# Performance work log

Measured on AMD Instinct MI355X. Metric: run time of the kernel, lower is better.

Reference implementation:

```python
import jax, jax.numpy as jnp
import numpy as np

HIDDEN = 1024
HEADS = 16
D_K = HIDDEN // HEADS
B, S = 2, 2048


def setup_inputs() -> dict:
    key = jax.random.key(0)
    ks = jax.random.split(key, 11)
    sc = 1.0 / np.sqrt(HIDDEN)
    inp = {
        "q": jax.random.normal(ks[0], (B, S, HIDDEN), jnp.float32),
        "k": jax.random.normal(ks[1], (B, S, HIDDEN), jnp.float32),
        "v": jax.random.normal(ks[2], (B, S, HIDDEN), jnp.float32),
        "Wq": jax.random.normal(ks[3], (HIDDEN, HIDDEN), jnp.float32) * sc,
        "bq": jnp.zeros((HIDDEN,), jnp.float32),
        "Wk": jax.random.normal(ks[4], (HIDDEN, HIDDEN), jnp.float32) * sc,
        "bk": jnp.zeros((HIDDEN,), jnp.float32),
        "Wv": jax.random.normal(ks[5], (HIDDEN, HIDDEN), jnp.float32) * sc,
        "bv": jnp.zeros((HIDDEN,), jnp.float32),
        "Wo": jax.random.normal(ks[6], (HIDDEN, HIDDEN), jnp.float32) * sc,
        "bo": jnp.zeros((HIDDEN,), jnp.float32),
    }
    return inp


def reference(q, k, v, Wq, bq, Wk, bk, Wv, bv, Wo, bo):
    bs = q.shape[0]
    # projections; torch Linear: x @ W.T + b
    def proj(x, W, b):
        y = x @ W.T + b  # [B,S,H*Dk]
        return y.reshape(bs, -1, HEADS, D_K).transpose(0, 2, 1, 3)  # [B,h,S,Dk]
    qh, kh, vh = proj(q, Wq, bq), proj(k, Wk, bk), proj(v, Wv, bv)
    scores = jnp.einsum("bhqd,bhkd->bhqk", qh, kh) / jnp.sqrt(jnp.float32(D_K))
    attn = jax.nn.softmax(scores, axis=-1)  # dropout is identity in eval mode
    x = jnp.einsum("bhqk,bhkd->bhqd", attn, vh)
    x = x.transpose(0, 2, 1, 3).reshape(bs, -1, HEADS * D_K)
    return x @ Wo.T + bo
```

## Files before the change

kernel.cpp:

```cpp
#include <hip/hip_runtime.h>
#include <stdint.h>

#define HIDDEN 1024
#define HEADS  16
#define DK     64
#define BATCH  2
#define SEQ    2048
#define MTOT   (BATCH*SEQ)
#define QSCALE 0.1803368801111204f

typedef float  f32x4   __attribute__((ext_vector_type(4)));
typedef float  f32x16  __attribute__((ext_vector_type(16)));
typedef __bf16 bf16x8  __attribute__((ext_vector_type(8)));

__device__ __forceinline__ unsigned short f2bf(float f) {
    union { float f; uint32_t u; } x;
    x.f = f;
    uint32_t r = x.u + 0x7fffu + ((x.u >> 16) & 1u);
    return (unsigned short)(r >> 16);
}

__device__ __forceinline__ bf16x8 ld_bf8(const unsigned short* p) {
    return *reinterpret_cast<const bf16x8*>(p);
}

__device__ __forceinline__ void gload16(const void* g, void* l) {
    __builtin_amdgcn_global_load_lds(
        (const __attribute__((address_space(1))) void*)g,
        (__attribute__((address_space(3))) void*)l, 16, 0, 0);
}

__device__ __forceinline__ uint32_t pkbf(float a, float b) {
    union { __bf16 h[2]; uint32_t u; } pk;
    pk.h[0] = (__bf16)a; pk.h[1] = (__bf16)b;
    return pk.u;
}

__device__ __forceinline__ float tsum16(const f32x16& v) {
    float a = (v[0] + v[1]) + (v[2] + v[3]);
    float b = (v[4] + v[5]) + (v[6] + v[7]);
    float c = (v[8] + v[9]) + (v[10] + v[11]);
    float d = (v[12] + v[13]) + (v[14] + v[15]);
    return (a + b) + (c + d);
}

struct Cvt7 {
    const float* s[7];
    unsigned short* d[7];
    int n8[7];
};
__global__ __launch_bounds__(256) void cvt_all(Cvt7 a) {
    int id = blockIdx.y;
    int i = blockIdx.x * blockDim.x + threadIdx.x;
    if (i >= a.n8[id]) return;
    const float4* s = reinterpret_cast<const float4*>(a.s[id]) + (size_t)i * 2;
    float4 x = s[0], y = s[1];
    union { unsigned short us[8]; uint4 v; } o;
    o.us[0] = f2bf(x.x); o.us[1] = f2bf(x.y); o.us[2] = f2bf(x.z); o.us[3] = f2bf(x.w);
    o.us[4] = f2bf(y.x); o.us[5] = f2bf(y.y); o.us[6] = f2bf(y.z); o.us[7] = f2bf(y.w);
    reinterpret_cast<uint4*>(a.d[id])[i] = o.v;
}

__device__ __forceinline__ void gemm_body(const unsigned short* __restrict__ A,
                                          const unsigned short* __restrict__ W,
                                          const float* __restrict__ bias,
                                          void* __restrict__ out, int mode, float scale,
                                          int bm, int bn) {
    __shared__ __align__(16) unsigned short Alds[2][128 * 64];
    __shared__ __align__(16) unsigned short Blds[2][128 * 64];
    const int t    = threadIdx.x;
    const int lane = t & 63;
    const int wid  = t >> 6;
    const int wm   = (wid >> 1) * 64;
    const int wn   = (wid & 1) * 64;
    const int fr   = lane & 15;
    const int fg   = lane >> 4;
    const int K    = HIDDEN;

    f32x4 acc[4][4];
#pragma unroll
    for (int i = 0; i < 4; i++)
#pragma unroll
        for (int j = 0; j < 4; j++) acc[i][j] = (f32x4){0.f, 0.f, 0.f, 0.f};

    const int seg_row = t >> 3;
    const int seg_col = ((t & 7) ^ (seg_row & 7)) * 8;
    const int ldst    = (t & ~63) * 8;

    const unsigned short* ga = A + (size_t)(bm * 128 + seg_row) * K + seg_col;
    const unsigned short* gb = W + (size_t)(bn * 128 + seg_row) * K + seg_col;

    auto stage = [&](int k0, int buf) {
#pragma unroll
        for (int i = 0; i < 4; i++) {
            gload16(ga + (size_t)(i * 32) * K + k0, &Alds[buf][i * 2048 + ldst]);
            gload16(gb + (size_t)(i * 32) * K + k0, &Blds[buf][i * 2048 + ldst]);
        }
    };

    stage(0, 0);
    __syncthreads();

    for (int ks = 0; ks < K / 64; ++ks) {
        const int cur = ks & 1;
        if (ks < K / 64 - 1) stage((ks + 1) * 64, cur ^ 1);
#pragma unroll
        for (int kk = 0; kk < 2; kk++) {
            bf16x8 af[4], bf[4];
#pragma unroll
            for (int mt = 0; mt < 4; mt++)
                af[mt] = ld_bf8(&Alds[cur][(wm + mt * 16 + fr) * 64 +
                                           (((kk * 4 + fg) ^ (fr & 7)) * 8)]);
#pragma unroll
            for (int nt = 0; nt < 4; nt++)
                bf[nt] = ld_bf8(&Blds[cur][(wn + nt * 16 + fr) * 64 +
                                           (((kk * 4 + fg) ^ (fr & 7)) * 8)]);
#pragma unroll
            for (int mt = 0; mt < 4; mt++)
#pragma unroll
                for (int nt = 0; nt < 4; nt++)
                    acc[mt][nt] = __builtin_amdgcn_mfma_f32_16x16x32_bf16(
                        af[mt], bf[nt], acc[mt][nt], 0, 0, 0);
        }
        __syncthreads();
    }

    const int base_row = bm * 128 + wm + fg * 4;
    const int base_col = bn * 128 + wn + fr;
#pragma unroll
    for (int mt = 0; mt < 4; mt++) {
#pragma unroll
        for (int nt = 0; nt < 4; nt++) {
            int col = base_col + nt * 16;
            float bv = bias[col];
            if (mode == 1) {
                int row0 = base_row + mt * 16;
                int b = row0 >> 11, s = row0 & (SEQ - 1);
                int h = col >> 6, d = col & (DK - 1);
                union { unsigned short us[4]; uint2 v; } pk;
#pragma unroll
                for (int e = 0; e < 4; e++)
                    pk.us[e] = f2bf((acc[mt][nt][e] + bv) * scale);
                *reinterpret_cast<uint2*>(
                    (unsigned short*)out + ((size_t)(b * HEADS + h) * DK + d) * SEQ + s) = pk.v;
            } else {
#pragma unroll
                for (int e = 0; e < 4; e++) {
                    int row = base_row + mt * 16 + e;
                    float val = (acc[mt][nt][e] + bv) * scale;
                    if (mode == 2) {
                        ((float*)out)[(size_t)row * HIDDEN + col] = val;
                    } else {
                        int b = row >> 11, s = row & (SEQ - 1);
                        int h = col >> 6, d = col & (DK - 1);
                        ((unsigned short*)out)[((size_t)(b * HEADS + h) * SEQ + s) * DK + d] =
                            f2bf(val);
                    }
                }
            }
        }
    }
}

__device__ __forceinline__ void xcd_swz(int bx, int by, int& bm, int& bn) {
    int lin = by * 8 + bx;
    int xcd = lin & 7;
    int idx = lin >> 3;
    bm = xcd * 4 + (idx >> 3);
    bn = idx & 7;
}

__global__ __launch_bounds__(256) void gemm_qkv(
    const unsigned short* __restrict__ qbf, const unsigned short* __restrict__ kbf,
    const unsigned short* __restrict__ vbf, const unsigned short* __restrict__ wq,
    const unsigned short* __restrict__ wk, const unsigned short* __restrict__ wv,
    const float* __restrict__ bq, const float* __restrict__ bk,
    const float* __restrict__ bv, unsigned short* __restrict__ qh,
    unsigned short* __restrict__ kh, unsigned short* __restrict__ vt) {
    int z = blockIdx.z;
    const unsigned short* A = (z == 0) ? qbf : (z == 1) ? kbf : vbf;
    const unsigned short* W = (z == 0) ? wq : (z == 1) ? wk : wv;
    const float* bias       = (z == 0) ? bq : (z == 1) ? bk : bv;
    unsigned short* out     = (z == 0) ? qh : (z == 1) ? kh : vt;
    int bm, bn;
    xcd_swz(blockIdx.x, blockIdx.y, bm, bn);
    gemm_body(A, W, bias, out, (z == 2) ? 1 : 0, (z == 0) ? QSCALE : 1.0f, bm, bn);
}

__global__ __launch_bounds__(256) void gemm_out(const unsigned short* __restrict__ ctx,
                                                const unsigned short* __restrict__ wo,
                                                const float* __restrict__ bo,
                                                float* __restrict__ out) {
    int bm, bn;
    xcd_swz(blockIdx.x, blockIdx.y, bm, bn);
    gemm_body(ctx, wo, bo, out, 2, 1.0f, bm, bn);
}

__global__ __launch_bounds__(512, 8) void attn_kernel(const unsigned short* __restrict__ qh,
                                                      const unsigned short* __restrict__ kh,
                                                      const unsigned short* __restrict__ vt,
                                                      unsigned short* __restrict__ ctx) {
    const int t = threadIdx.x, lane = t & 63, w = t >> 6;
    const int lo = lane & 31, hi = lane >> 5;
    const int qsub = w & 3, split = w >> 2;
    const int id = blockIdx.x;
    const int g  = (id & 7) * 64 + (id >> 3);
    const int by = g >> 4;
    const int bx = g & 15;
    const size_t hb = (size_t)by * (SEQ * DK);
    const int q0 = bx * 128 + qsub * 32;

    struct KV { unsigned short K[2][2][64 * 64]; unsigned short V[2][2][64 * 64]; };
    struct MG { float Lo[4][32][64]; float Ll[4][64]; };
    __shared__ union SMem { KV kv; MG mg; } sm;

    const unsigned short* sp[4];
    unsigned short* dpK[4];
    int sstr[4];
#pragma unroll
    for (int i = 0; i < 4; ++i) {
        int u   = w * 4 + i;
        int isV = u >> 4;
        int ssp = (u >> 3) & 1;
        int r0  = (u & 7) * 8;
        int rl  = r0 + (lane >> 3);
        int cs  = ((lane & 7) ^ ((lane >> 3) & 7)) * 8;
        if (!isV) {
            sp[i]   = kh + hb + (size_t)(ssp * 1024 + rl) * DK + cs;
            sstr[i] = 64 * DK;
            dpK[i]  = &sm.kv.K[0][ssp][r0 * 64];
        } else {
            sp[i]   = vt + hb + (size_t)rl * SEQ + ssp * 1024 + cs;
            sstr[i] = 64;
            dpK[i]  = &sm.kv.V[0][ssp][r0 * 64];
        }
    }
    const int bufoff = 2 * 64 * 64;

    bf16x8 qf[4];
#pragma unroll
    for (int tl = 0; tl < 4; ++tl)
        qf[tl] = ld_bf8(&qh[hb + (size_t)(q0 + lo) * DK + tl * 16 + hi * 8]);

    f32x16 o0, o1;
#pragma unroll
    for (int e = 0; e < 16; ++e) { o0[e] = 0.f; o1[e] = 0.f; }
    float l = 0.f;

#pragma unroll
    for (int i = 0; i < 4; ++i) { gload16(sp[i], dpK[i]); sp[i] += sstr[i]; }
    __syncthreads();

    const int xr = lo & 7;

    for (int it = 0; it < 16; ++it) {
        const unsigned short* Kb = &sm.kv.K[it & 1][split][0];
        const unsigned short* Vb = &sm.kv.V[it & 1][split][0];
        if (it < 15) {
#pragma unroll
            for (int i = 0; i < 4; ++i) {
                unsigned short* d = dpK[i] + ((it & 1) ? 0 : bufoff);
                gload16(sp[i], d);
                sp[i] += sstr[i];
            }
        }
        f32x16 sA, sB;
#pragma unroll
        for (int e = 0; e < 16; ++e) { sA[e] = 0.f; sB[e] = 0.f; }
        __builtin_amdgcn_s_setprio(1);
#pragma unroll
        for (int tl = 0; tl < 4; ++tl) {
            int c = 2 * tl + hi;
            bf16x8 kfA = ld_bf8(&Kb[lo * 64 + ((c ^ xr) * 8)]);
            bf16x8 kfB = ld_bf8(&Kb[(32 + lo) * 64 + ((c ^ xr) * 8)]);
            sA = __builtin_amdgcn_mfma_f32_32x32x16_bf16(kfA, qf[tl], sA, 0, 0, 0);
            sB = __builtin_amdgcn_mfma_f32_32x32x16_bf16(kfB, qf[tl], sB, 0, 0, 0);
        }
        __builtin_amdgcn_s_setprio(0);
#pragma unroll
        for (int e = 0; e < 16; ++e) {
            sA[e] = __builtin_amdgcn_exp2f(sA[e]);
            sB[e] = __builtin_amdgcn_exp2f(sB[e]);
        }
        {
            float sum = tsum16(sA) + tsum16(sB);
            sum += __shfl_xor(sum, 32);
            l += sum;
        }
        uint32_t pA[8], pB[8];
#pragma unroll
        for (int i = 0; i < 8; ++i) {
            pA[i] = pkbf(sA[2 * i], sA[2 * i + 1]);
            pB[i] = pkbf(sB[2 * i], sB[2 * i + 1]);
        }
        asm volatile("v_permlane32_swap_b32 %0, %1" : "+v"(pA[0]), "+v"(pA[2]));
        asm volatile("v_permlane32_swap_b32 %0, %1" : "+v"(pA[1]), "+v"(pA[3]));
        asm volatile("v_permlane32_swap_b32 %0, %1" : "+v"(pA[4]), "+v"(pA[6]));
        asm volatile("v_permlane32_swap_b32 %0, %1" : "+v"(pA[5]), "+v"(pA[7]));
        asm volatile("v_permlane32_swap_b32 %0, %1" : "+v"(pB[0]), "+v"(pB[2]));
        asm volatile("v_permlane32_swap_b32 %0, %1" : "+v"(pB[1]), "+v"(pB[3]));
        asm volatile("v_permlane32_swap_b32 %0, %1" : "+v"(pB[4]), "+v"(pB[6]));
        asm volatile("v_permlane32_swap_b32 %0, %1" : "+v"(pB[5]), "+v"(pB[7]));
        union { uint32_t u[4]; bf16x8 v; } f0, f1, f2, f3;
        f0.u[0] = pA[0]; f0.u[1] = pA[1]; f0.u[2] = pA[2]; f0.u[3] = pA[3];
        f1.u[0] = pA[4]; f1.u[1] = pA[5]; f1.u[2] = pA[6]; f1.u[3] = pA[7];
        f2.u[0] = pB[0]; f2.u[1] = pB[1]; f2.u[2] = pB[2]; f2.u[3] = pB[3];
        f3.u[0] = pB[4]; f3.u[1] = pB[5]; f3.u[2] = pB[6]; f3.u[3] = pB[7];
        bf16x8 v00 = ld_bf8(&Vb[lo * 64 + (((0 + hi) ^ xr) * 8)]);
        bf16x8 v01 = ld_bf8(&Vb[lo * 64 + (((2 + hi) ^ xr) * 8)]);
        bf16x8 v02 = ld_bf8(&Vb[lo * 64 + (((4 + hi) ^ xr) * 8)]);
        bf16x8 v03 = ld_bf8(&Vb[lo * 64 + (((6 + hi) ^ xr) * 8)]);
        bf16x8 v10 = ld_bf8(&Vb[(32 + lo) * 64 + (((0 + hi) ^ xr) * 8)]);
        bf16x8 v11 = ld_bf8(&Vb[(32 + lo) * 64 + (((2 + hi) ^ xr) * 8)]);
        bf16x8 v12 = ld_bf8(&Vb[(32 + lo) * 64 + (((4 + hi) ^ xr) * 8)]);
        bf16x8 v13 = ld_bf8(&Vb[(32 + lo) * 64 + (((6 + hi) ^ xr) * 8)]);
        __builtin_amdgcn_s_setprio(1);
        o0 = __builtin_amdgcn_mfma_f32_32x32x16_bf16(v00, f0.v, o0, 0, 0, 0);
        o0 = __builtin_amdgcn_mfma_f32_32x32x16_bf16(v01, f1.v, o0, 0, 0, 0);
        o0 = __builtin_amdgcn_mfma_f32_32x32x16_bf16(v02, f2.v, o0, 0, 0, 0);
        o0 = __builtin_amdgcn_mfma_f32_32x32x16_bf16(v03, f3.v, o0, 0, 0, 0);
        o1 = __builtin_amdgcn_mfma_f32_32x32x16_bf16(v10, f0.v, o1, 0, 0, 0);
        o1 = __builtin_amdgcn_mfma_f32_32x32x16_bf16(v11, f1.v, o1, 0, 0, 0);
        o1 = __builtin_amdgcn_mfma_f32_32x32x16_bf16(v12, f2.v, o1, 0, 0, 0);
        o1 = __builtin_amdgcn_mfma_f32_32x32x16_bf16(v13, f3.v, o1, 0, 0, 0);
        __builtin_amdgcn_s_setprio(0);
        __syncthreads();
    }

    if (split == 1) {
#pragma unroll
        for (int e = 0; e < 16; ++e) {
            sm.mg.Lo[qsub][e][lane]      = o0[e];
            sm.mg.Lo[qsub][16 + e][lane] = o1[e];
        }
        sm.mg.Ll[qsub][lane] = l;
    }
    __syncthreads();
    if (split == 0) {
        const int b = by >> 4, hd = by & 15;
        float rl = __builtin_amdgcn_rcpf(l + sm.mg.Ll[qsub][lane]);
        unsigned short* orow = ctx + ((size_t)(b * SEQ + q0 + lo)) * HIDDEN + hd * 64;
#pragma unroll
        for (int dt = 0; dt < 2; ++dt) {
#pragma unroll
            for (int gq = 0; gq < 4; ++gq) {
                union { unsigned short us[4]; uint2 v; } pk;
#pragma unroll
                for (int c = 0; c < 4; ++c) {
                    int e = gq * 4 + c;
                    float own = dt ? o1[e] : o0[e];
                    float oth = sm.mg.Lo[qsub][dt * 16 + e][lane];
                    pk.us[c] = f2bf((own + oth) * rl);
                }
                *reinterpret_cast<uint2*>(orow + dt * 32 + gq * 8 + hi * 4) = pk.v;
            }
        }
    }
}

extern "C" void kernel_launch(void* const* d_in, const int* in_sizes, int n_in,
                              void* d_out, int out_size, void* d_ws, size_t ws_size,
                              hipStream_t stream) {
    const float* q  = (const float*)d_in[0];
    const float* k  = (const float*)d_in[1];
    const float* v  = (const float*)d_in[2];
    const float* Wq = (const float*)d_in[3];
    const float* bq = (const float*)d_in[4];
    const float* Wk = (const float*)d_in[5];
    const float* bk = (const float*)d_in[6];
    const float* Wv = (const float*)d_in[7];
    const float* bv = (const float*)d_in[8];
    const float* Wo = (const float*)d_in[9];
    const float* bo = (const float*)d_in[10];

    unsigned short* qbf = (unsigned short*)d_ws;
    unsigned short* kbf = qbf + (size_t)MTOT * HIDDEN;
    unsigned short* vbf = kbf + (size_t)MTOT * HIDDEN;
    unsigned short* wqb = vbf + (size_t)MTOT * HIDDEN;
    unsigned short* wkb = wqb + (size_t)HIDDEN * HIDDEN;
    unsigned short* wvb = wkb + (size_t)HIDDEN * HIDDEN;
    unsigned short* wob = wvb + (size_t)HIDDEN * HIDDEN;
    unsigned short* qh  = wob + (size_t)HIDDEN * HIDDEN;
    unsigned short* kh  = qh + (size_t)MTOT * HIDDEN;
    unsigned short* vt  = kh + (size_t)MTOT * HIDDEN;
    unsigned short* ctx = vt + (size_t)MTOT * HIDDEN;

    const int nAct8 = MTOT * HIDDEN / 8;
    const int nW8   = HIDDEN * HIDDEN / 8;

    Cvt7 ca;
    ca.s[0] = q;  ca.d[0] = qbf; ca.n8[0] = nAct8;
    ca.s[1] = k;  ca.d[1] = kbf; ca.n8[1] = nAct8;
    ca.s[2] = v;  ca.d[2] = vbf; ca.n8[2] = nAct8;
    ca.s[3] = Wq; ca.d[3] = wqb; ca.n8[3] = nW8;
    ca.s[4] = Wk; ca.d[4] = wkb; ca.n8[4] = nW8;
    ca.s[5] = Wv; ca.d[5] = wvb; ca.n8[5] = nW8;
    ca.s[6] = Wo; ca.d[6] = wob; ca.n8[6] = nW8;
    cvt_all<<<dim3(nAct8 / 256, 7), dim3(256), 0, stream>>>(ca);

    gemm_qkv<<<dim3(HIDDEN / 128, MTOT / 128, 3), dim3(256), 0, stream>>>(
        qbf, kbf, vbf, wqb, wkb, wvb, bq, bk, bv, qh, kh, vt);

    attn_kernel<<<dim3(512), dim3(512), 0, stream>>>(qh, kh, vt, ctx);

    gemm_out<<<dim3(HIDDEN / 128, MTOT / 128), dim3(256), 0, stream>>>(
        ctx, wob, bo, (float*)d_out);
}
```

Before: 131.8 us.

## Remove intra-block KV split in attention; use 4 waves over full sequence

The attention kernel drops its two-way split of the key/value sequence across wave groups. Blocks shrink from 512 to 256 threads, and each wave now loops over all 32 KV tiles instead of 16. This removes the shared-memory merge of partial outputs, its extra barrier and the larger LDS union, and halves the per-block LDS footprint. In exchange each wave runs twice as many serial iterations, with less latency hiding per block, and the softmax normalisation no longer sums partial denominators.

```diff
diff --git a/kernel.cpp b/kernel.cpp
--- a/kernel.cpp
+++ b/kernel.cpp
@@ -196,23 +196,21 @@
     gemm_body(ctx, wo, bo, out, 2, 1.0f, bm, bn);
 }
 
-__global__ __launch_bounds__(512, 8) void attn_kernel(const unsigned short* __restrict__ qh,
+__global__ __launch_bounds__(256, 4) void attn_kernel(const unsigned short* __restrict__ qh,
                                                       const unsigned short* __restrict__ kh,
                                                       const unsigned short* __restrict__ vt,
                                                       unsigned short* __restrict__ ctx) {
     const int t = threadIdx.x, lane = t & 63, w = t >> 6;
     const int lo = lane & 31, hi = lane >> 5;
-    const int qsub = w & 3, split = w >> 2;
     const int id = blockIdx.x;
     const int g  = (id & 7) * 64 + (id >> 3);
     const int by = g >> 4;
     const int bx = g & 15;
     const size_t hb = (size_t)by * (SEQ * DK);
-    const int q0 = bx * 128 + qsub * 32;
-
-    struct KV { unsigned short K[2][2][64 * 64]; unsigned short V[2][2][64 * 64]; };
-    struct MG { float Lo[4][32][64]; float Ll[4][64]; };
-    __shared__ union SMem { KV kv; MG mg; } sm;
+    const int q0 = bx * 128 + w * 32;
+
+    __shared__ __align__(16) unsigned short Klds[2][64 * 64];
+    __shared__ __align__(16) unsigned short Vlds[2][64 * 64];
 
     const unsigned short* sp[4];
     unsigned short* dpK[4];
@@ -220,22 +218,21 @@
 #pragma unroll
     for (int i = 0; i < 4; ++i) {
         int u   = w * 4 + i;
-        int isV = u >> 4;
-        int ssp = (u >> 3) & 1;
+        int isV = u >> 3;
         int r0  = (u & 7) * 8;
         int rl  = r0 + (lane >> 3);
         int cs  = ((lane & 7) ^ ((lane >> 3) & 7)) * 8;
         if (!isV) {
-            sp[i]   = kh + hb + (size_t)(ssp * 1024 + rl) * DK + cs;
+            sp[i]   = kh + hb + (size_t)rl * DK + cs;
             sstr[i] = 64 * DK;
-            dpK[i]  = &sm.kv.K[0][ssp][r0 * 64];
+            dpK[i]  = &Klds[0][r0 * 64];
         } else {
-            sp[i]   = vt + hb + (size_t)rl * SEQ + ssp * 1024 + cs;
+            sp[i]   = vt + hb + (size_t)rl * SEQ + cs;
             sstr[i] = 64;
-            dpK[i]  = &sm.kv.V[0][ssp][r0 * 64];
-        }
-    }
-    const int bufoff = 2 * 64 * 64;
+            dpK[i]  = &Vlds[0][r0 * 64];
+        }
+    }
+    const int bufoff = 64 * 64;
 
     bf16x8 qf[4];
 #pragma unroll
@@ -253,10 +250,10 @@
 
     const int xr = lo & 7;
 
-    for (int it = 0; it < 16; ++it) {
-        const unsigned short* Kb = &sm.kv.K[it & 1][split][0];
-        const unsigned short* Vb = &sm.kv.V[it & 1][split][0];
-        if (it < 15) {
+    for (int it = 0; it < 32; ++it) {
+        const unsigned short* Kb = &Klds[it & 1][0];
+        const unsigned short* Vb = &Vlds[it & 1][0];
+        if (it < 31) {
 #pragma unroll
             for (int i = 0; i < 4; ++i) {
                 unsigned short* d = dpK[i] + ((it & 1) ? 0 : bufoff);
@@ -327,33 +324,21 @@
         __syncthreads();
     }
 
-    if (split == 1) {
-#pragma unroll
-        for (int e = 0; e < 16; ++e) {
-            sm.mg.Lo[qsub][e][lane]      = o0[e];
-            sm.mg.Lo[qsub][16 + e][lane] = o1[e];
-        }
-        sm.mg.Ll[qsub][lane] = l;
-    }
-    __syncthreads();
-    if (split == 0) {
-        const int b = by >> 4, hd = by & 15;
-        float rl = __builtin_amdgcn_rcpf(l + sm.mg.Ll[qsub][lane]);
-        unsigned short* orow = ctx + ((size_t)(b * SEQ + q0 + lo)) * HIDDEN + hd * 64;
-#pragma unroll
-        for (int dt = 0; dt < 2; ++dt) {
-#pragma unroll
-            for (int gq = 0; gq < 4; ++gq) {
-                union { unsigned short us[4]; uint2 v; } pk;
-#pragma unroll
-                for (int c = 0; c < 4; ++c) {
-                    int e = gq * 4 + c;
-                    float own = dt ? o1[e] : o0[e];
-                    float oth = sm.mg.Lo[qsub][dt * 16 + e][lane];
-                    pk.us[c] = f2bf((own + oth) * rl);
-                }
-                *reinterpret_cast<uint2*>(orow + dt * 32 + gq * 8 + hi * 4) = pk.v;
+    const int b = by >> 4, hd = by & 15;
+    float rl = __builtin_amdgcn_rcpf(l);
+    unsigned short* orow = ctx + ((size_t)(b * SEQ + q0 + lo)) * HIDDEN + hd * 64;
+#pragma unroll
+    for (int dt = 0; dt < 2; ++dt) {
+#pragma unroll
+        for (int gq = 0; gq < 4; ++gq) {
+            union { unsigned short us[4]; uint2 v; } pk;
+#pragma unroll
+            for (int c = 0; c < 4; ++c) {
+                int e = gq * 4 + c;
+                float own = dt ? o1[e] : o0[e];
+                pk.us[c] = f2bf(own * rl);
             }
+            *reinterpret_cast<uint2*>(orow + dt * 32 + gq * 8 + hi * 4) = pk.v;
         }
     }
 }
@@ -401,7 +386,7 @@
     gemm_qkv<<<dim3(HIDDEN / 128, MTOT / 128, 3), dim3(256), 0, stream>>>(
         qbf, kbf, vbf, wqb, wkb, wvb, bq, bk, bv, qh, kh, vt);
 
-    attn_kernel<<<dim3(512), dim3(512), 0, stream>>>(qh, kh, vt, ctx);
+    attn_kernel<<<dim3(512), dim3(256), 0, stream>>>(qh, kh, vt, ctx);
 
     gemm_out<<<dim3(HIDDEN / 128, MTOT / 128), dim3(256), 0, stream>>>(
         ctx, wob, bo, (float*)d_out);
```

Measured after the change: 131.9 us. About the same (+0.1%).
